# Optimization experiments

Hardware: AMD Instinct MI355X
Metric: run time of the kernel (lower is better)

The kernel has to match this reference:

```python
import jax, jax.numpy as jnp
import numpy as np

N = 768          # number of nodes (points)
F = 128          # n_invariant_feat_hidden (0e channels)
V = 64           # n_vectors_hidden (1e channels)
S_RO, V_RO = 128, 64   # readout_mlp_irreps widths
S_OUT, V_OUT = 64, 32  # output_irreps widths
R_HID = 16       # radial MLP hidden width
AVG = 64.0       # avg_num_neighbors normalization
N_LAYERS = 2     # num_interactions


def _w(key, shape):
    fan_in = shape[-2] if len(shape) > 1 else 1
    return jax.random.normal(key, shape, jnp.float32) / np.sqrt(fan_in)


def setup_inputs() -> dict:
    key = jax.random.key(0)
    ks = jax.random.split(key, 16)
    x = jax.random.normal(ks[0], (N, 3), jnp.float32) * 2.0
    idx = np.arange(N)
    s, r = np.meshgrid(idx, idx, indexing='ij')
    mask = s != r  # fully connected graph, no self edges
    senders = jnp.asarray(s[mask], jnp.int32)
    receivers = jnp.asarray(r[mask], jnp.int32)
    return {
        'x': x,
        'senders': senders,
        'receivers': receivers,
        'embed': _w(ks[1], (1, F)),            # species embedding (num_species=1)
        'Wr1': _w(ks[2], (N_LAYERS, 1, R_HID)),
        'Wr2s': _w(ks[3], (N_LAYERS, R_HID, F)),
        'Wr2v': _w(ks[4], (N_LAYERS, R_HID, V)),
        'Wsv': _w(ks[5], (N_LAYERS, F, V)),
        'Wss': _w(ks[6], (N_LAYERS, F, F)),
        'Wvs': _w(ks[7], (N_LAYERS, V, F)),
        'Wvv': _w(ks[8], (N_LAYERS, V, V)),
        'Wro_s1': _w(ks[9], (F, S_RO)),
        'Wro_s2': _w(ks[10], (S_RO, S_OUT)),
        'Wro_v1': _w(ks[11], (V, V_RO)),
        'Wro_v2': _w(ks[12], (V_RO, V_OUT)),
    }


def reference(x, senders, receivers, embed, Wr1, Wr2s, Wr2v, Wsv, Wss, Wvs, Wvv,
              Wro_s1, Wro_s2, Wro_v1, Wro_v2):
    n = x.shape[0]
    vec = x[senders] - x[receivers]                 # [E, 3] pairwise displacement
    d = jnp.linalg.norm(vec, axis=-1, keepdims=True)  # [E, 1] radial basis (identity)
    sh1 = vec / (d + 1e-8)                          # l=1 spherical harmonics (unit vector)

    hs = jnp.broadcast_to(embed[0], (n, F))         # node_specie == 0 for all nodes
    hv = jnp.zeros((n, V, 3), x.dtype)

    for l in range(N_LAYERS):
        rf = jax.nn.silu(d @ Wr1[l])                # [E, R_HID] radial MLP
        ws = rf @ Wr2s[l]                           # [E, F] scalar path radial weights
        wv = rf @ Wr2v[l]                           # [E, V] vector path radial weights
        hs_e = hs[senders]                          # gather sender scalars [E, F]
        m_s = hs_e * ws                             # 0e x 0e -> 0e messages
        m_v = ((hs_e @ Wsv[l]) * wv)[:, :, None] * sh1[:, None, :]  # 0e x 1e -> 1e [E,V,3]
        agg_s = jax.ops.segment_sum(m_s, receivers, num_segments=n) / AVG
        agg_v = jax.ops.segment_sum(m_v, receivers, num_segments=n) / AVG
        inv = jnp.sum(agg_v * agg_v, axis=-1)       # 1e (x) 1e -> 0e contraction [N, V]
        hs = jax.nn.silu(hs + agg_s @ Wss[l] + inv @ Wvs[l])
        hv = hv + jnp.einsum('nvd,vw->nwd', agg_v, Wvv[l])

    ro_s = jax.nn.silu(hs @ Wro_s1) @ Wro_s2        # [N, S_OUT]
    ro_v = jnp.einsum('nvd,vw->nwd',
                      jnp.einsum('nvd,vw->nwd', hv, Wro_v1), Wro_v2)  # [N, V_OUT, 3]
    return jnp.concatenate([ro_s, ro_v.reshape(n, -1)], axis=-1)       # [N, S_OUT + 3*V_OUT]
```

## Files before the change

### kernel.cpp

```cpp
#include <hip/hip_runtime.h>
#include <hip/hip_bf16.h>
#include <math.h>

#define NN 768
#define FF 128
#define VV 64
#define RH 16
#define SPLITK 24
#define SEND_PER_KC 32
#define NITER 4
#define KSTEPS 384
#define NT_S 8
#define NT_V 16
#define MB_N 24
#define CHUNK 256
#define RPAD 260

typedef __attribute__((ext_vector_type(8))) short bf16x8_t;
typedef __attribute__((ext_vector_type(4))) float f32x4;

__device__ __forceinline__ float silu_f(float a) {
  return a * __builtin_amdgcn_rcpf(1.0f + __expf(-a));
}

__device__ __forceinline__ short f2bf(float f) {
  __hip_bfloat16 h = __float2bfloat16(f);
  return __builtin_bit_cast(short, h);
}

__device__ __forceinline__ float bf2f(unsigned short v) {
  return __builtin_bit_cast(float, (unsigned)v << 16);
}

__global__ __launch_bounds__(256) void layer0_kernel(
    const float* __restrict__ x,
    const float* __restrict__ Wr1,
    const float* __restrict__ Wr2s,
    const float* __restrict__ Wr2v,
    const float* __restrict__ embed,
    const float* __restrict__ Wsv0,
    const float* __restrict__ Wss,
    const float* __restrict__ Wvs,
    const float* __restrict__ Wvv,
    const float* __restrict__ Wsv1,
    float* __restrict__ hs,
    float* __restrict__ hsv,
    float* __restrict__ hv)
{
  __shared__ float rf_t[RH * RPAD];
  __shared__ float u_t[4 * RPAD];
  __shared__ float red[4][64];
  __shared__ float fin[64];
  __shared__ float cvs[64];
  __shared__ float as_l[FF];
  __shared__ float av_l[192];
  __shared__ float inv_l[VV];
  __shared__ float hsn[FF];
  __shared__ float redn[256];

  const int r   = blockIdx.x;
  const int tid = threadIdx.x;
  const int j   = tid & 63;
  const int q   = tid >> 6;
  const int h   = j >> 2;
  const int c   = j & 3;
  const int sel = (c + 3) & 3;

  if (tid < 64) {
    float a = 0.f;
    #pragma unroll 8
    for (int f = 0; f < FF; ++f) a += embed[f] * Wsv0[f * VV + tid];
    cvs[tid] = a;
  }

  float wr1[RH];
  #pragma unroll
  for (int hh = 0; hh < RH; ++hh) wr1[hh] = Wr1[hh];

  const float xr0 = x[r * 3 + 0], xr1 = x[r * 3 + 1], xr2 = x[r * 3 + 2];

  float acc = 0.f;
  for (int cb = 0; cb < NN; cb += CHUNK) {
    {
      const int s = cb + tid;
      const float vx = x[s * 3 + 0] - xr0;
      const float vy = x[s * 3 + 1] - xr1;
      const float vz = x[s * 3 + 2] - xr2;
      const float d  = __builtin_amdgcn_sqrtf(vx * vx + vy * vy + vz * vz);
      const float iv = __builtin_amdgcn_rcpf(d + 1e-8f);
      u_t[0 * RPAD + tid] = vx * iv;
      u_t[1 * RPAD + tid] = vy * iv;
      u_t[2 * RPAD + tid] = vz * iv;
      u_t[3 * RPAD + tid] = 1.0f;
      #pragma unroll
      for (int hh = 0; hh < RH; ++hh)
        rf_t[hh * RPAD + tid] = silu_f(d * wr1[hh]);
    }
    __syncthreads();

    const float* rp = &rf_t[h * RPAD + q * 64];
    const float* up = &u_t[sel * RPAD + q * 64];
    #pragma unroll 8
    for (int si = 0; si < 64; si += 4) {
      const float4 ra = *(const float4*)&rp[si];
      const float4 ua = *(const float4*)&up[si];
      acc += ra.x * ua.x + ra.y * ua.y + ra.z * ua.z + ra.w * ua.w;
    }
    __syncthreads();
  }

  red[q][j] = acc;
  __syncthreads();
  if (tid < 64) fin[tid] = red[0][tid] + red[1][tid] + red[2][tid] + red[3][tid];
  __syncthreads();

  if (tid < FF) {
    float a = 0.f;
    #pragma unroll
    for (int hh = 0; hh < RH; ++hh) a += fin[hh * 4] * Wr2s[hh * FF + tid];
    as_l[tid] = a * embed[tid] * (1.0f / 64.0f);
  }
  if (tid < 192) {
    const int v = tid / 3, d = tid - v * 3;
    float a = 0.f;
    #pragma unroll
    for (int hh = 0; hh < RH; ++hh) a += fin[hh * 4 + 1 + d] * Wr2v[hh * VV + v];
    av_l[tid] = a * cvs[v] * (1.0f / 64.0f);
  }
  __syncthreads();

  if (tid < VV) {
    const float a0 = av_l[tid * 3 + 0], a1 = av_l[tid * 3 + 1], a2 = av_l[tid * 3 + 2];
    inv_l[tid] = a0 * a0 + a1 * a1 + a2 * a2;
  }
  __syncthreads();

  {
    const int f = tid & 127, part = tid >> 7;
    float a = 0.f;
    const float* wp = Wss + (part * 64) * FF + f;
    #pragma unroll 8
    for (int kk = 0; kk < 64; ++kk) a += as_l[part * 64 + kk] * wp[kk * FF];
    const float* vp = Wvs + (part * 32) * FF + f;
    #pragma unroll 8
    for (int vv = 0; vv < 32; ++vv) a += inv_l[part * 32 + vv] * vp[vv * FF];
    redn[part * 128 + f] = a;
  }
  __syncthreads();

  if (tid < FF) {
    const float hnew = silu_f(embed[tid] + redn[tid] + redn[128 + tid]);
    hs[(size_t)r * FF + tid] = hnew;
    hsn[tid] = hnew;
  }
  if (tid < 192) {
    const int w = tid / 3, d = tid - w * 3;
    float a = 0.f;
    #pragma unroll 8
    for (int v = 0; v < VV; ++v) a += av_l[v * 3 + d] * Wvv[v * VV + w];
    hv[(size_t)r * 192 + tid] = a;
  }
  __syncthreads();

  {
    const int v = tid & 63, part = tid >> 6;
    float a = 0.f;
    const float* wp = Wsv1 + (part * 32) * VV + v;
    #pragma unroll 8
    for (int f = 0; f < 32; ++f) a += hsn[part * 32 + f] * wp[f * VV];
    redn[tid] = a;
  }
  __syncthreads();
  if (tid < VV)
    hsv[(size_t)r * VV + tid] = redn[tid] + redn[64 + tid] + redn[128 + tid] + redn[192 + tid];
}

__global__ __launch_bounds__(256) void prep_kernel(
    const float* __restrict__ hs, const float* __restrict__ hsv,
    const float* __restrict__ x,
    const float* __restrict__ Wr2s,
    const float* __restrict__ Wr2v,
    unsigned short* __restrict__ Bs, unsigned short* __restrict__ Bv)
{
  const int gid   = blockIdx.x * 256 + threadIdx.x;
  const int lane  = gid & 63;
  const int tmp   = gid >> 6;
  const int ntile = tmp % 24;
  const int kstep = tmp / 24;
  if (kstep >= KSTEPS) return;
  const int qq = lane >> 4;
  const int s  = kstep * 2 + (qq >> 1);
  const int hb = (qq & 1) * 8;

  bf16x8_t o;
  if (ntile < NT_S) {
    const int f = ntile * 16 + (lane & 15);
    const float hf = hs[s * FF + f] * 0.015625f;
    #pragma unroll
    for (int e = 0; e < 8; ++e)
      o[e] = f2bf(hf * Wr2s[(hb + e) * FF + f]);
    *(bf16x8_t*)&Bs[((size_t)(kstep * NT_S + ntile) * 64 + lane) * 8] = o;
  } else {
    const int nt2 = ntile - NT_S;
    const int n   = nt2 * 16 + (lane & 15);
    int v; float scale;
    if (n < 192) { const int dd = n >> 6; v = n & 63;
                   scale = x[s * 3 + dd] * hsv[s * VV + v] * 0.015625f; }
    else         { v = n - 192; scale = hsv[s * VV + v] * 0.015625f; }
    #pragma unroll
    for (int e = 0; e < 8; ++e)
      o[e] = f2bf(scale * Wr2v[(hb + e) * VV + v]);
    *(bf16x8_t*)&Bv[((size_t)(kstep * NT_V + nt2) * 64 + lane) * 8] = o;
  }
}

__global__ __launch_bounds__(256) void edge_gemm(
    const float* __restrict__ x,
    const unsigned short* __restrict__ Bs,
    const unsigned short* __restrict__ Bv,
    const float* __restrict__ Wr1,
    unsigned short* __restrict__ Ps,
    unsigned short* __restrict__ Pv)
{
  __shared__ unsigned short A_lds[4 * 2 * 64 * 8];
  __shared__ unsigned short G_lds[4 * 2 * 64 * 8];

  const int wg = ((blockIdx.x & 7) * 72) + (blockIdx.x >> 3);
  const int kc = wg / MB_N;
  const int mb = wg - kc * MB_N;

  const int tid  = threadIdx.x;
  const int lane = tid & 63;
  const int w    = tid >> 6;

  float wr1[RH];
  #pragma unroll
  for (int h = 0; h < RH; ++h) wr1[h] = Wr1[h];

  const int r_local = tid & 31;
  const int s_ii    = tid >> 5;
  const int r = mb * 32 + r_local;
  const int mt_w  = r_local >> 4;
  const int ks_w  = s_ii >> 1;
  const int lane0 = (r_local & 15) + ((s_ii & 1) << 5);

  const float xr0 = x[r * 3 + 0], xr1 = x[r * 3 + 1], xr2 = x[r * 3 + 2];
  float sx[NITER], sy[NITER], sz[NITER];
  #pragma unroll
  for (int it = 0; it < NITER; ++it) {
    const int s = kc * SEND_PER_KC + it * 8 + s_ii;
    sx[it] = x[s * 3 + 0]; sy[it] = x[s * 3 + 1]; sz[it] = x[s * 3 + 2];
  }

  f32x4 accS[4], accV[8];
  #pragma unroll
  for (int i = 0; i < 4; ++i) accS[i] = (f32x4){0.f, 0.f, 0.f, 0.f};
  #pragma unroll
  for (int i = 0; i < 8; ++i) accV[i] = (f32x4){0.f, 0.f, 0.f, 0.f};

  for (int it = 0; it < NITER; ++it) {
    {
      const float vx = sx[it] - xr0;
      const float vy = sy[it] - xr1;
      const float vz = sz[it] - xr2;
      const float dd = __builtin_amdgcn_sqrtf(vx * vx + vy * vy + vz * vz);
      const float iv = __builtin_amdgcn_rcpf(dd + 1e-8f);
      float sv[RH];
      #pragma unroll
      for (int h = 0; h < RH; ++h) sv[h] = silu_f(dd * wr1[h]);
      bf16x8_t o0, o1, g0, g1;
      #pragma unroll
      for (int h = 0; h < 8; ++h) {
        o0[h] = f2bf(sv[h]);
        o1[h] = f2bf(sv[h + 8]);
        g0[h] = f2bf(sv[h] * iv);
        g1[h] = f2bf(sv[h + 8] * iv);
      }
      const int off0 = ((ks_w * 2 + mt_w) * 64 + lane0) * 8;
      *(bf16x8_t*)&A_lds[off0]       = o0;
      *(bf16x8_t*)&A_lds[off0 + 128] = o1;
      *(bf16x8_t*)&G_lds[off0]       = g0;
      *(bf16x8_t*)&G_lds[off0 + 128] = g1;
    }
    __syncthreads();

    const int kgb = kc * (SEND_PER_KC / 2) + it * 4;
    #pragma unroll
    for (int ks = 0; ks < 4; ++ks) {
      const bf16x8_t b0 =
          *(const bf16x8_t*)&Bs[((size_t)((kgb + ks) * NT_S + 2 * w) * 64 + lane) * 8];
      const bf16x8_t b1 =
          *(const bf16x8_t*)&Bs[((size_t)((kgb + ks) * NT_S + 2 * w + 1) * 64 + lane) * 8];
      bf16x8_t bv[4];
      #pragma unroll
      for (int j = 0; j < 4; ++j)
        bv[j] = *(const bf16x8_t*)&Bv[((size_t)((kgb + ks) * NT_V + 4 * w + j) * 64 + lane) * 8];
      #pragma unroll
      for (int mt = 0; mt < 2; ++mt) {
        const int aoff = ((ks * 2 + mt) * 64 + lane) * 8;
        const bf16x8_t a  = *(const bf16x8_t*)&A_lds[aoff];
        const bf16x8_t ag = *(const bf16x8_t*)&G_lds[aoff];
        accS[mt * 2 + 0] = __builtin_amdgcn_mfma_f32_16x16x32_bf16(a, b0, accS[mt * 2 + 0], 0, 0, 0);
        accS[mt * 2 + 1] = __builtin_amdgcn_mfma_f32_16x16x32_bf16(a, b1, accS[mt * 2 + 1], 0, 0, 0);
        #pragma unroll
        for (int j = 0; j < 4; ++j)
          accV[mt * 4 + j] = __builtin_amdgcn_mfma_f32_16x16x32_bf16(ag, bv[j], accV[mt * 4 + j], 0, 0, 0);
      }
    }
    __syncthreads();
  }

  const int rowq = (lane >> 4) << 2;
  #pragma unroll
  for (int j = 0; j < 2; ++j) {
    const int col = (2 * w + j) * 16 + (lane & 15);
    #pragma unroll
    for (int mt = 0; mt < 2; ++mt) {
      #pragma unroll
      for (int reg = 0; reg < 4; ++reg) {
        const int row = mb * 32 + mt * 16 + rowq + reg;
        Ps[((size_t)kc * NN + row) * FF + col] =
            (unsigned short)f2bf(accS[mt * 2 + j][reg]);
      }
    }
  }
  #pragma unroll
  for (int j = 0; j < 4; ++j) {
    const int col = (4 * w + j) * 16 + (lane & 15);
    #pragma unroll
    for (int mt = 0; mt < 2; ++mt) {
      #pragma unroll
      for (int reg = 0; reg < 4; ++reg) {
        const int row = mb * 32 + mt * 16 + rowq + reg;
        Pv[((size_t)kc * NN + row) * 256 + col] =
            (unsigned short)f2bf(accV[mt * 4 + j][reg]);
      }
    }
  }
}

__global__ __launch_bounds__(512) void final_kernel(
    const unsigned short* __restrict__ Ps,
    const unsigned short* __restrict__ Pv,
    const float* __restrict__ x,
    const float* __restrict__ hs,
    const float* __restrict__ hv,
    const float* __restrict__ Wss,
    const float* __restrict__ Wvs,
    const float* __restrict__ Wvv,
    const float* __restrict__ Wro_s1,
    const float* __restrict__ Wro_s2,
    const float* __restrict__ Wro_v1,
    const float* __restrict__ Wro_v2,
    float* __restrict__ out)
{
  __shared__ float as_l[FF];
  __shared__ float pvs_l[256];
  __shared__ float av_l[192];
  __shared__ float inv_l[VV];
  __shared__ float hsn[FF];
  __shared__ float hv_l[192];
  __shared__ float red[512];
  __shared__ float red2[384];
  __shared__ float t1[FF];
  __shared__ float tv1[192];
  const int n = blockIdx.x, t = threadIdx.x;

  if (t < FF) {
    float a = 0.f;
    #pragma unroll
    for (int kc = 0; kc < SPLITK; ++kc)
      a += bf2f(Ps[((size_t)kc * NN + n) * FF + t]);
    as_l[t] = a;
  } else if (t < 384) {
    const int cc = t - 128;
    float a = 0.f;
    #pragma unroll
    for (int kc = 0; kc < SPLITK; ++kc)
      a += bf2f(Pv[((size_t)kc * NN + n) * 256 + cc]);
    pvs_l[cc] = a;
  }
  __syncthreads();

  if (t < VV) {
    const float base = pvs_l[192 + t];
    const float a0 = pvs_l[t]       - x[n * 3 + 0] * base;
    const float a1 = pvs_l[64 + t]  - x[n * 3 + 1] * base;
    const float a2 = pvs_l[128 + t] - x[n * 3 + 2] * base;
    av_l[t * 3 + 0] = a0; av_l[t * 3 + 1] = a1; av_l[t * 3 + 2] = a2;
    inv_l[t] = a0 * a0 + a1 * a1 + a2 * a2;
  }
  __syncthreads();

  {
    const int f = t & 127, part = t >> 7;
    float acc = 0.f;
    const float* wp = Wss + (part * 32) * FF + f;
    #pragma unroll 8
    for (int kk = 0; kk < 32; ++kk) acc += as_l[part * 32 + kk] * wp[kk * FF];
    const float* vp = Wvs + (part * 16) * FF + f;
    #pragma unroll 8
    for (int vv = 0; vv < 16; ++vv) acc += inv_l[part * 16 + vv] * vp[vv * FF];
    red[part * 128 + f] = acc;
  }
  __syncthreads();

  if (t < FF) {
    hsn[t] = silu_f(hs[n * FF + t] + red[t] + red[128 + t] + red[256 + t] + red[384 + t]);
  }
  if (t < 384) {
    const int part = t / 192, j = t - part * 192;
    const int wv = j / 3, d = j - wv * 3;
    float acc = 0.f;
    const float* vp = Wvv + (part * 32) * VV + wv;
    #pragma unroll 8
    for (int v = 0; v < 32; ++v) acc += av_l[(part * 32 + v) * 3 + d] * vp[v * VV];
    red2[part * 192 + j] = acc;
  }
  __syncthreads();

  if (t < 192) hv_l[t] = hv[n * 192 + t] + red2[t] + red2[192 + t];
  __syncthreads();

  {
    const int f = t & 127, part = t >> 7;
    float acc = 0.f;
    const float* wp = Wro_s1 + (part * 32) * FF + f;
    #pragma unroll 8
    for (int kk = 0; kk < 32; ++kk) acc += hsn[part * 32 + kk] * wp[kk * FF];
    red[part * 128 + f] = acc;
  }
  __syncthreads();
  if (t < FF) t1[t] = silu_f(red[t] + red[128 + t] + red[256 + t] + red[384 + t]);
  if (t < 384) {
    const int part = t / 192, j = t - part * 192;
    const int wv = j / 3, d = j - wv * 3;
    float acc = 0.f;
    const float* vp = Wro_v1 + (part * 32) * VV + wv;
    #pragma unroll 8
    for (int v = 0; v < 32; ++v) acc += hv_l[(part * 32 + v) * 3 + d] * vp[v * VV];
    red2[part * 192 + j] = acc;
  }
  __syncthreads();
  if (t < 192) tv1[t] = red2[t] + red2[192 + t];
  if (t < 256) {
    const int o = t & 63, part = t >> 6;
    float acc = 0.f;
    const float* wp = Wro_s2 + (part * 32) * 64 + o;
    #pragma unroll 8
    for (int f = 0; f < 32; ++f) acc += t1[part * 32 + f] * wp[f * 64];
    red[t] = acc;
  }
  __syncthreads();
  if (t < 64) out[n * 160 + t] = red[t] + red[64 + t] + red[128 + t] + red[192 + t];
  if (t < 192) {
    const int part = t / 96, j = t - part * 96;
    const int w2 = j / 3, d = j - w2 * 3;
    float acc = 0.f;
    const float* vp = Wro_v2 + (part * 32) * 32 + w2;
    #pragma unroll 8
    for (int wv = 0; wv < 32; ++wv) acc += tv1[(part * 32 + wv) * 3 + d] * vp[wv * 32];
    red2[part * 96 + j] = acc;
  }
  __syncthreads();
  if (t < 96) out[n * 160 + 64 + t] = red2[t] + red2[96 + t];
}

extern "C" void kernel_launch(void* const* d_in, const int* in_sizes, int n_in,
                              void* d_out, int out_size, void* d_ws, size_t ws_size,
                              hipStream_t stream) {
  const float* x      = (const float*)d_in[0];
  const float* embed  = (const float*)d_in[3];
  const float* Wr1    = (const float*)d_in[4];
  const float* Wr2s   = (const float*)d_in[5];
  const float* Wr2v   = (const float*)d_in[6];
  const float* Wsv    = (const float*)d_in[7];
  const float* Wss    = (const float*)d_in[8];
  const float* Wvs    = (const float*)d_in[9];
  const float* Wvv    = (const float*)d_in[10];
  const float* Wro_s1 = (const float*)d_in[11];
  const float* Wro_s2 = (const float*)d_in[12];
  const float* Wro_v1 = (const float*)d_in[13];
  const float* Wro_v2 = (const float*)d_in[14];

  float* ws_f = (float*)d_ws;
  float* hs    = ws_f;
  float* hsv   = hs + NN * FF;
  float* hv    = hsv + NN * VV;
  unsigned short* Ps = (unsigned short*)(hv + NN * 192);
  unsigned short* Pv = Ps + (size_t)SPLITK * NN * FF;
  unsigned short* Bs = Pv + (size_t)SPLITK * NN * 256;
  unsigned short* Bv = Bs + (size_t)12288 * 128;
  float* out = (float*)d_out;

  layer0_kernel<<<NN, 256, 0, stream>>>(
      x, Wr1, Wr2s, Wr2v, embed, Wsv, Wss, Wvs, Wvv, Wsv + FF * VV,
      hs, hsv, hv);

  prep_kernel<<<2304, 256, 0, stream>>>(
      hs, hsv, x, Wr2s + RH * FF, Wr2v + RH * VV, Bs, Bv);
  edge_gemm<<<MB_N * SPLITK, 256, 0, stream>>>(
      x, Bs, Bv, Wr1 + RH, Ps, Pv);
  final_kernel<<<NN, 512, 0, stream>>>(
      Ps, Pv, x, hs, hv, Wss + FF * FF, Wvs + VV * FF, Wvv + VV * VV,
      Wro_s1, Wro_s2, Wro_v1, Wro_v2, out);
}
```

Baseline: 61.12 us.

## Accumulate radial moments per thread in registers and reduce via padded LDS transpose

Layer-0 radial/direction moments were computed by staging rf and unit vectors in LDS per 256-sender chunk, with each thread then doing dot products. Now each thread processes 3 senders, accumulating all 64 moment sums (16 hidden × {1,x,y,z}) in registers, then reduces across threads through a padded 33-stride LDS transpose in two halves. This removes the chunked LDS staging and repeated syncs but uses 64 accumulator registers and a larger shared buffer.

Result: faster. 58.77 us (-3.8%).

```diff
diff --git a/kernel.cpp b/kernel.cpp
--- a/kernel.cpp
+++ b/kernel.cpp
@@ -13,8 +13,6 @@
 #define NT_S 8
 #define NT_V 16
 #define MB_N 24
-#define CHUNK 256
-#define RPAD 260
 
 typedef __attribute__((ext_vector_type(8))) short bf16x8_t;
 typedef __attribute__((ext_vector_type(4))) float f32x4;
@@ -47,9 +45,8 @@
     float* __restrict__ hsv,
     float* __restrict__ hv)
 {
-  __shared__ float rf_t[RH * RPAD];
-  __shared__ float u_t[4 * RPAD];
-  __shared__ float red[4][64];
+  __shared__ float accT[256 * 33];
+  __shared__ float red8[8][32];
   __shared__ float fin[64];
   __shared__ float cvs[64];
   __shared__ float as_l[FF];
@@ -60,11 +57,6 @@
 
   const int r   = blockIdx.x;
   const int tid = threadIdx.x;
-  const int j   = tid & 63;
-  const int q   = tid >> 6;
-  const int h   = j >> 2;
-  const int c   = j & 3;
-  const int sel = (c + 3) & 3;
 
   if (tid < 64) {
     float a = 0.f;
@@ -79,40 +71,74 @@
 
   const float xr0 = x[r * 3 + 0], xr1 = x[r * 3 + 1], xr2 = x[r * 3 + 2];
 
-  float acc = 0.f;
-  for (int cb = 0; cb < NN; cb += CHUNK) {
+  float acc[64];
+  #pragma unroll
+  for (int i = 0; i < 64; ++i) acc[i] = 0.f;
+
+  #pragma unroll
+  for (int ss = 0; ss < 3; ++ss) {
+    const int s = tid + ss * 256;
+    const float vx = x[s * 3 + 0] - xr0;
+    const float vy = x[s * 3 + 1] - xr1;
+    const float vz = x[s * 3 + 2] - xr2;
+    const float d  = __builtin_amdgcn_sqrtf(vx * vx + vy * vy + vz * vz);
+    const float iv = __builtin_amdgcn_rcpf(d + 1e-8f);
+    const float ux = vx * iv, uy = vy * iv, uz = vz * iv;
+    #pragma unroll
+    for (int h = 0; h < RH; ++h) {
+      const float rf = silu_f(d * wr1[h]);
+      acc[h * 4 + 0] += rf;
+      acc[h * 4 + 1] += rf * ux;
+      acc[h * 4 + 2] += rf * uy;
+      acc[h * 4 + 3] += rf * uz;
+    }
+  }
+
+  {
+    #pragma unroll
+    for (int i = 0; i < 32; ++i) accT[tid * 33 + i] = acc[i];
+    __syncthreads();
     {
-      const int s = cb + tid;
-      const float vx = x[s * 3 + 0] - xr0;
-      const float vy = x[s * 3 + 1] - xr1;
-      const float vz = x[s * 3 + 2] - xr2;
-      const float d  = __builtin_amdgcn_sqrtf(vx * vx + vy * vy + vz * vz);
-      const float iv = __builtin_amdgcn_rcpf(d + 1e-8f);
-      u_t[0 * RPAD + tid] = vx * iv;
-      u_t[1 * RPAD + tid] = vy * iv;
-      u_t[2 * RPAD + tid] = vz * iv;
-      u_t[3 * RPAD + tid] = 1.0f;
-      #pragma unroll
-      for (int hh = 0; hh < RH; ++hh)
-        rf_t[hh * RPAD + tid] = silu_f(d * wr1[hh]);
-    }
-    __syncthreads();
-
-    const float* rp = &rf_t[h * RPAD + q * 64];
-    const float* up = &u_t[sel * RPAD + q * 64];
-    #pragma unroll 8
-    for (int si = 0; si < 64; si += 4) {
-      const float4 ra = *(const float4*)&rp[si];
-      const float4 ua = *(const float4*)&up[si];
-      acc += ra.x * ua.x + ra.y * ua.y + ra.z * ua.z + ra.w * ua.w;
-    }
-    __syncthreads();
-  }
-
-  red[q][j] = acc;
-  __syncthreads();
-  if (tid < 64) fin[tid] = red[0][tid] + red[1][tid] + red[2][tid] + red[3][tid];
-  __syncthreads();
+      const int j2 = tid & 31, q2 = tid >> 5;
+      float a0 = 0.f, a1 = 0.f;
+      #pragma unroll 8
+      for (int rr = 0; rr < 32; rr += 2) {
+        a0 += accT[(q2 * 32 + rr) * 33 + j2];
+        a1 += accT[(q2 * 32 + rr + 1) * 33 + j2];
+      }
+      red8[q2][j2] = a0 + a1;
+    }
+    __syncthreads();
+    if (tid < 32) {
+      float a = 0.f;
+      #pragma unroll
+      for (int g = 0; g < 8; ++g) a += red8[g][tid];
+      fin[tid] = a;
+    }
+    __syncthreads();
+
+    #pragma unroll
+    for (int i = 0; i < 32; ++i) accT[tid * 33 + i] = acc[32 + i];
+    __syncthreads();
+    {
+      const int j2 = tid & 31, q2 = tid >> 5;
+      float a0 = 0.f, a1 = 0.f;
+      #pragma unroll 8
+      for (int rr = 0; rr < 32; rr += 2) {
+        a0 += accT[(q2 * 32 + rr) * 33 + j2];
+        a1 += accT[(q2 * 32 + rr + 1) * 33 + j2];
+      }
+      red8[q2][j2] = a0 + a1;
+    }
+    __syncthreads();
+    if (tid < 32) {
+      float a = 0.f;
+      #pragma unroll
+      for (int g = 0; g < 8; ++g) a += red8[g][tid];
+      fin[32 + tid] = a;
+    }
+    __syncthreads();
+  }
 
   if (tid < FF) {
     float a = 0.f;
```
